# Kernel optimization log

Measured on AMD Instinct MI355X. Metric: run time of the kernel, lower is better.

Reference implementation:

```python
import jax, jax.numpy as jnp
import numpy as np

K_MASK = -2.3819763e+38
ROPE_THETA = 1000000
MROPE_SECTION = (24, 20, 20)
NORM_EPS = 1e-6


def rms_norm(x, w, eps=NORM_EPS):
    dtype = x.dtype
    x32 = x.astype(jnp.float32)
    rms_inv = jax.lax.rsqrt(jnp.mean(x32 * x32, axis=-1, keepdims=True) + eps)
    return w * (x32 * rms_inv).astype(dtype)


def apply_rope(inputs, positions, head_dim, rope_theta=ROPE_THETA, mrope_section=MROPE_SECTION):
    # positions: [3, B, T] (temporal, height, width); inputs: [B, T, heads, head_dim]
    fraction = 2 * jnp.arange(0, head_dim // 2, dtype=jnp.float32) / head_dim
    timescale = rope_theta ** fraction  # [head_dim//2]
    sinusoid = positions[:, :, :, None].astype(jnp.float32) / timescale  # [3,B,T,hd/2]
    freq = sinusoid[0]
    h_idx = jnp.arange(1, mrope_section[1] * 3, 3)
    w_idx = jnp.arange(2, mrope_section[2] * 3, 3)
    freq = freq.at[..., h_idx].set(sinusoid[1][..., h_idx])
    freq = freq.at[..., w_idx].set(sinusoid[2][..., w_idx])
    freq = freq[:, :, None, :]  # [B,T,1,hd/2]
    sin, cos = jnp.sin(freq), jnp.cos(freq)
    first, second = jnp.split(inputs, 2, axis=-1)
    out = jnp.concatenate([first * cos - second * sin, second * cos + first * sin], axis=-1)
    return out.astype(inputs.dtype)


def setup_inputs() -> dict:
    key = jax.random.key(0)
    ks = jax.random.split(key, 6)
    B, T, D, N, K, H = 2, 1024, 2560, 32, 8, 128
    x = jax.random.normal(ks[0], (B, T, D), dtype=jnp.float32)
    positions = jnp.broadcast_to(jnp.arange(T, dtype=jnp.int32), (3, B, T))
    attn_mask = jnp.tril(jnp.ones((T, T), dtype=bool))[None].repeat(B, axis=0)  # causal [B,T,T]
    wq = jax.random.normal(ks[1], (D, N, H), dtype=jnp.float32) * 0.02
    wk = jax.random.normal(ks[2], (D, K, H), dtype=jnp.float32) * 0.02
    wv = jax.random.normal(ks[3], (D, K, H), dtype=jnp.float32) * 0.02
    wo = jax.random.normal(ks[4], (N, H, D), dtype=jnp.float32) * 0.02
    q_norm_w = jnp.ones((H,), dtype=jnp.float32)
    k_norm_w = jnp.ones((H,), dtype=jnp.float32)
    return {"x": x, "positions": positions, "attn_mask": attn_mask, "wq": wq,
            "wk": wk, "wv": wv, "wo": wo, "q_norm_w": q_norm_w, "k_norm_w": k_norm_w}


def reference(x, positions, attn_mask, wq, wk, wv, wo, q_norm_w, k_norm_w):
    head_dim = wo.shape[1]
    scale = head_dim ** -0.5
    q = rms_norm(jnp.einsum('btd,dnh->btnh', x, wq), q_norm_w)
    k = rms_norm(jnp.einsum('bsd,dkh->bskh', x, wk), k_norm_w)
    v = jnp.einsum('bsd,dkh->bskh', x, wv)
    q = apply_rope(q, positions, head_dim)
    k = apply_rope(k, positions, head_dim)
    b, t, qh, d = q.shape
    _, s, kh, _ = k.shape
    q = q.reshape((b, t, kh, qh // kh, d))  # GQA grouping
    attn = jnp.einsum('bthgd,bshd->bhgts', q, k) * scale
    attn = attn.reshape((b, qh, t, s))
    attn = jnp.where(attn_mask[:, None, :, :], attn, K_MASK)
    attn = jax.nn.softmax(attn.astype(jnp.float32), axis=-1).astype(k.dtype)
    attn = attn.reshape((b, kh, qh // kh, t, s))
    qkv = jnp.einsum('bhgts,bshd->bthgd', attn, v).reshape((b, t, qh, d))
    return jnp.einsum('btnh,nhd->btd', qkv, wo)
```

## Files before the change

### kernel.cpp

```cpp
#include <hip/hip_runtime.h>
#include <hip/hip_bf16.h>

typedef __attribute__((ext_vector_type(8))) __bf16 bf8_t;
typedef __attribute__((ext_vector_type(4))) float f32x4;
typedef __attribute__((ext_vector_type(16))) float f32x16;

#define GLOAD16(gptr, lptr)                                                              \
  __builtin_amdgcn_global_load_lds((const __attribute__((address_space(1))) void*)(gptr), \
                                   (__attribute__((address_space(3))) void*)(lptr), 16, 0, 0)

__device__ __forceinline__ unsigned short f2bf(float f) {
  union { float f; unsigned u; } v; v.f = f;
  return (unsigned short)((v.u + 0x7fffu + ((v.u >> 16) & 1u)) >> 16);
}

__device__ __forceinline__ unsigned cvtpk_bf16(float a, float b) {
  unsigned r;
  asm("v_cvt_pk_bf16_f32 %0, %1, %2" : "=v"(r) : "v"(a), "v"(b));
  return r;
}

__global__ void cast_bf16(const float* __restrict__ in, unsigned short* __restrict__ out, int n4) {
  int i = blockIdx.x * blockDim.x + threadIdx.x;
  if (i >= n4) return;
  float4 v = ((const float4*)in)[i];
  ushort4 o;
  o.x = f2bf(v.x); o.y = f2bf(v.y); o.z = f2bf(v.z); o.w = f2bf(v.w);
  ((ushort4*)out)[i] = o;
}

__global__ void tcast(const float* __restrict__ in, unsigned short* __restrict__ out,
                      int R, int C, int ld, int rowOff) {
  __shared__ float tile[32][33];
  int c0 = blockIdx.x * 32, r0 = blockIdx.y * 32;
  int tx = threadIdx.x, ty = threadIdx.y;
#pragma unroll
  for (int i = 0; i < 4; ++i)
    tile[ty + 8 * i][tx] = in[(size_t)(r0 + ty + 8 * i) * C + c0 + tx];
  __syncthreads();
#pragma unroll
  for (int i = 0; i < 4; ++i)
    out[(size_t)(rowOff + c0 + ty + 8 * i) * ld + r0 + tx] = f2bf(tile[tx][ty + 8 * i]);
}

__global__ __launch_bounds__(512, 2) void gemm256(
    const unsigned short* __restrict__ A,
    const unsigned short* __restrict__ Bt,
    float* __restrict__ C0, float* __restrict__ C1,
    int N, int ldk, int Kslice, int nTileN) {
  __shared__ unsigned short SM[4][2][8192];
  int ks = blockIdx.y;
  float* __restrict__ C = ks ? C1 : C0;
  int kbase = ks * Kslice;
  int bm = blockIdx.x / nTileN, bn = blockIdx.x % nTileN;
  int m0 = bm << 8, n0 = bn << 8;
  int tid = threadIdx.x, lane = tid & 63, w = tid >> 6;
  int wm = w >> 2, wn = w & 3;
  int lrow = lane & 15, lch = lane >> 4;
  int srow = tid >> 2, scol = (tid & 3) << 3;
  int nt = Kslice >> 5;

  f32x4 acc[8][4] = {};

  auto stage = [&](int t) {
    int buf = t & 3;
    int k0 = kbase + (t << 5);
    const unsigned short* Ag = A + (size_t)(m0 + srow) * ldk + k0 + scol;
    const unsigned short* Bg = Bt + (size_t)(n0 + srow) * ldk + k0 + scol;
    unsigned short* Al = &SM[buf][0][w << 9];
    unsigned short* Bl = &SM[buf][1][w << 9];
    GLOAD16(Ag, Al);
    GLOAD16(Ag + (size_t)128 * ldk, Al + 4096);
    GLOAD16(Bg, Bl);
    GLOAD16(Bg + (size_t)128 * ldk, Bl + 4096);
  };

  stage(0);
  stage(1);
  for (int t = 0; t < nt; ++t) {
    if (t + 2 < nt) stage(t + 2);
    if (t + 2 < nt)      asm volatile("s_waitcnt vmcnt(8)" ::: "memory");
    else if (t + 1 < nt) asm volatile("s_waitcnt vmcnt(4)" ::: "memory");
    else                 asm volatile("s_waitcnt vmcnt(0)" ::: "memory");
    asm volatile("s_barrier" ::: "memory");
    int buf = t & 3;
    const unsigned short* As = &SM[buf][0][0];
    const unsigned short* Bs = &SM[buf][1][0];
    bf8_t a[8], b[4];
#pragma unroll
    for (int mi = 0; mi < 8; ++mi)
      a[mi] = *(const bf8_t*)(As + ((wm << 7) + (mi << 4) + lrow) * 32 + (lch << 3));
#pragma unroll
    for (int ni = 0; ni < 4; ++ni)
      b[ni] = *(const bf8_t*)(Bs + ((wn << 6) + (ni << 4) + lrow) * 32 + (lch << 3));
    __builtin_amdgcn_s_setprio(1);
#pragma unroll
    for (int mi = 0; mi < 8; ++mi)
#pragma unroll
      for (int ni = 0; ni < 4; ++ni)
        acc[mi][ni] = __builtin_amdgcn_mfma_f32_16x16x32_bf16(a[mi], b[ni], acc[mi][ni], 0, 0, 0);
    __builtin_amdgcn_s_setprio(0);
  }
  int r0 = m0 + (wm << 7) + (lch << 2);
  int c0 = n0 + (wn << 6) + lrow;
#pragma unroll
  for (int mi = 0; mi < 8; ++mi)
#pragma unroll
    for (int ni = 0; ni < 4; ++ni)
#pragma unroll
      for (int r = 0; r < 4; ++r)
        C[(size_t)(r0 + (mi << 4) + r) * N + c0 + (ni << 4)] = acc[mi][ni][r];
}

__global__ void reduce_add(const float4* __restrict__ a, const float4* __restrict__ b,
                           float4* __restrict__ o, int n4) {
  int i = blockIdx.x * blockDim.x + threadIdx.x;
  if (i >= n4) return;
  float4 x = a[i], y = b[i];
  o[i] = make_float4(x.x + y.x, x.y + y.y, x.z + y.z, x.w + y.w);
}

__global__ __launch_bounds__(128) void normrope(
    const float* __restrict__ qkv, const int* __restrict__ positions,
    const float* __restrict__ qw, const float* __restrict__ kw,
    unsigned short* __restrict__ qb, unsigned short* __restrict__ kb,
    unsigned short* __restrict__ vt) {
  int blk = blockIdx.x;
  int hh = blk % 48, bt = blk / 48;
  int b = bt >> 10, t = bt & 1023;
  int tid = threadIdx.x;
  int colbase = (hh < 32) ? (hh << 7) : ((hh < 40) ? (4096 + ((hh - 32) << 7)) : (5120 + ((hh - 40) << 7)));
  float val = qkv[(size_t)bt * 6144 + colbase + tid];
  if (hh >= 40) {
    vt[((size_t)((b * 8 + hh - 40) * 128 + tid)) * 1024 + t] = f2bf(val);
    return;
  }
  __shared__ float red[2];
  __shared__ float xs[128];
  float ss = val * val;
#pragma unroll
  for (int m = 32; m >= 1; m >>= 1) ss += __shfl_xor(ss, m);
  if ((tid & 63) == 0) red[tid >> 6] = ss;
  __syncthreads();
  float rinv = rsqrtf((red[0] + red[1]) * (1.0f / 128.0f) + 1e-6f);
  float wgt = (hh < 32) ? qw[tid] : kw[tid];
  float xn = val * rinv * wgt;
  xs[tid] = xn;
  __syncthreads();
  float other = xs[tid ^ 64];
  int pos = positions[b * 1024 + t];
  int j = tid & 63;
  float ang = (float)pos * exp2f(-(float)j * 0.31143075889569027f);
  float sv = sinf(ang), cv = cosf(ang);
  float outv = (tid < 64) ? (xn * cv - other * sv) : (xn * cv + other * sv);
  unsigned short o = f2bf(outv);
  if (hh < 32) qb[((size_t)((b * 32 + hh) * 1024 + t)) * 128 + tid] = o;
  else kb[((size_t)((b * 8 + hh - 32) * 1024 + t)) * 128 + tid] = o;
}

__global__ __launch_bounds__(256, 2) void attn(
    const unsigned short* __restrict__ qb,
    const unsigned short* __restrict__ kb,
    const unsigned short* __restrict__ vt,
    unsigned short* __restrict__ ob) {
  __shared__ unsigned short Kl[2][64 * 128];
  __shared__ unsigned short Vl[2][128 * 64];
  int bx = blockIdx.x, hq = blockIdx.y, b = blockIdx.z;
  int qt = (bx < 4) ? (7 - bx) : (bx - 4);
  int kvh = hq >> 2;
  int tid = threadIdx.x, lane = tid & 63, w = tid >> 6;
  int qlane = lane & 31, h = lane >> 5;
  int q0 = (qt << 7) + (w << 5);
  int qg = q0 + qlane;
  const unsigned short* kbase = kb + ((size_t)(b * 8 + kvh) << 17);
  const unsigned short* vbase = vt + ((size_t)(b * 8 + kvh) << 17);
  const float c2 = 0.12751744f;

  const unsigned short* qptr = qb + ((size_t)((b * 32 + hq) * 1024 + qg) << 7) + (h << 3);
  bf8_t qf[8];
#pragma unroll
  for (int ds = 0; ds < 8; ++ds) qf[ds] = *(const bf8_t*)(qptr + ds * 16);

  f32x16 o[4] = {};
  float mrun = -3.0e38f, lrun = 0.f;
  int last_st = (q0 + 31) >> 6;
  int nsteps = 2 * qt + 2;

  auto stage = [&](int st, int buf) {
    int s0 = st << 6;
    unsigned short* kd = &Kl[buf][0];
    unsigned short* vd = &Vl[buf][0];
#pragma unroll
    for (int i = 0; i < 4; ++i) {
      int cid = i * 256 + tid;
      int kr = cid >> 4, ksl = cid & 15;
      GLOAD16(kbase + (size_t)(s0 + kr) * 128 + ((ksl ^ (kr & 15)) << 3), kd + cid * 8);
      int vr = cid >> 3, vsl = cid & 7;
      GLOAD16(vbase + (size_t)vr * 1024 + s0 + ((vsl ^ (vr & 7)) << 3), vd + cid * 8);
    }
  };

  stage(0, 0);
  for (int st = 0; st < nsteps; ++st) {
    __syncthreads();
    if (st + 1 < nsteps) stage(st + 1, (st + 1) & 1);
    if (st <= last_st) {
      const char* Kb = (const char*)&Kl[st & 1][0];
      const char* Vb = (const char*)&Vl[st & 1][0];
      f32x16 s0v = {}, s1v = {};
#pragma unroll
      for (int ds = 0; ds < 8; ++ds) {
        int c = ds * 2 + h;
        int r0 = qlane, r1 = 32 + qlane;
        bf8_t k0 = *(const bf8_t*)(Kb + r0 * 256 + ((c ^ (r0 & 15)) << 4));
        bf8_t k1 = *(const bf8_t*)(Kb + r1 * 256 + ((c ^ (r1 & 15)) << 4));
        s0v = __builtin_amdgcn_mfma_f32_32x32x16_bf16(k0, qf[ds], s0v, 0, 0, 0);
        s1v = __builtin_amdgcn_mfma_f32_32x32x16_bf16(k1, qf[ds], s1v, 0, 0, 0);
      }
      bool dm = (st == last_st);
      int kg0 = st << 6;
      float mt = -3.0e38f;
#pragma unroll
      for (int e = 0; e < 16; ++e) {
        int kl = (e & 3) + 8 * (e >> 2) + 4 * h;
        if (dm) {
          if (kg0 + kl > qg) s0v[e] = -3.0e38f;
          if (kg0 + 32 + kl > qg) s1v[e] = -3.0e38f;
        }
        mt = fmaxf(mt, fmaxf(s0v[e], s1v[e]));
      }
      mt = fmaxf(mt, __shfl_xor(mt, 32));
      float mnew = fmaxf(mrun, mt);
      float alpha = exp2f((mrun - mnew) * c2);
      float ls = 0.f;
#pragma unroll
      for (int e = 0; e < 16; ++e) {
        s0v[e] = exp2f((s0v[e] - mnew) * c2);
        s1v[e] = exp2f((s1v[e] - mnew) * c2);
        ls += s0v[e] + s1v[e];
      }
      ls += __shfl_xor(ls, 32);
      lrun = lrun * alpha + ls;
      mrun = mnew;
#pragma unroll
      for (int db = 0; db < 4; ++db)
#pragma unroll
        for (int e = 0; e < 16; ++e) o[db][e] *= alpha;
      bf8_t pf[4];
#pragma unroll
      for (int s = 0; s < 4; ++s) {
        unsigned w00, w01, w10, w11;
        {
          const int B0 = 4 * ((2 * s) & 3);
          if ((2 * s) >> 2) { w00 = cvtpk_bf16(s1v[B0], s1v[B0 + 1]); w01 = cvtpk_bf16(s1v[B0 + 2], s1v[B0 + 3]); }
          else              { w00 = cvtpk_bf16(s0v[B0], s0v[B0 + 1]); w01 = cvtpk_bf16(s0v[B0 + 2], s0v[B0 + 3]); }
        }
        {
          const int B1 = 4 * ((2 * s + 1) & 3);
          if ((2 * s + 1) >> 2) { w10 = cvtpk_bf16(s1v[B1], s1v[B1 + 1]); w11 = cvtpk_bf16(s1v[B1 + 2], s1v[B1 + 3]); }
          else                  { w10 = cvtpk_bf16(s0v[B1], s0v[B1 + 1]); w11 = cvtpk_bf16(s0v[B1 + 2], s0v[B1 + 3]); }
        }
        unsigned sa = h ? w00 : w10, sb = h ? w01 : w11;
        unsigned ra = __shfl_xor(sa, 32), rb = __shfl_xor(sb, 32);
        unsigned ka = h ? w10 : w00, kb2 = h ? w11 : w01;
        unsigned f0 = h ? ra : ka, f1 = h ? rb : kb2;
        unsigned f2 = h ? ka : ra, f3 = h ? kb2 : rb;
        uint4 fv = make_uint4(f0, f1, f2, f3);
        pf[s] = *(bf8_t*)&fv;
      }
#pragma unroll
      for (int db = 0; db < 4; ++db) {
        int vr = (db << 5) + qlane;
#pragma unroll
        for (int s = 0; s < 4; ++s) {
          int c = (s << 1) + h;
          bf8_t vf = *(const bf8_t*)(Vb + vr * 128 + ((c ^ (vr & 7)) << 4));
          o[db] = __builtin_amdgcn_mfma_f32_32x32x16_bf16(vf, pf[s], o[db], 0, 0, 0);
        }
      }
    }
  }

  __syncthreads();
  unsigned short* tb = &Kl[0][0] + (w << 12);
  float inv = 1.0f / lrun;
#pragma unroll
  for (int db = 0; db < 4; ++db)
#pragma unroll
    for (int rq = 0; rq < 4; ++rq) {
      int d0 = (db << 5) + (rq << 3) + (h << 2);
      unsigned lo = ((unsigned)f2bf(o[db][rq * 4 + 1] * inv) << 16) | f2bf(o[db][rq * 4 + 0] * inv);
      unsigned hi = ((unsigned)f2bf(o[db][rq * 4 + 3] * inv) << 16) | f2bf(o[db][rq * 4 + 2] * inv);
      *(uint2*)(tb + qlane * 128 + (d0 ^ ((qlane & 15) << 3))) = make_uint2(lo, hi);
    }
  int rr = lane >> 1, dh = (lane & 1) << 6;
  size_t orow = ((size_t)(b * 1024 + q0 + rr) << 12) + (hq << 7);
#pragma unroll
  for (int i = 0; i < 8; ++i) {
    int d8 = dh + i * 8;
    uint4 vv = *(const uint4*)(tb + rr * 128 + (d8 ^ ((rr & 15) << 3)));
    *(uint4*)(&ob[orow + d8]) = vv;
  }
}

extern "C" void kernel_launch(void* const* d_in, const int* in_sizes, int n_in,
                              void* d_out, int out_size, void* d_ws, size_t ws_size,
                              hipStream_t stream) {
  const float* x = (const float*)d_in[0];
  const int* positions = (const int*)d_in[1];
  const float* wq = (const float*)d_in[3];
  const float* wk = (const float*)d_in[4];
  const float* wv = (const float*)d_in[5];
  const float* wo = (const float*)d_in[6];
  const float* qnw = (const float*)d_in[7];
  const float* knw = (const float*)d_in[8];
  float* out = (float*)d_out;

  char* ws = (char*)d_ws;
  unsigned short* x_bf  = (unsigned short*)(ws);
  unsigned short* wqkvT = (unsigned short*)(ws + 10485760);
  unsigned short* woT   = (unsigned short*)(ws + 41943040);
  float*          qkv   = (float*)(ws + 62914560);
  float*          p0    = (float*)(ws + 62914560);
  float*          p1    = (float*)(ws + 83886080);
  unsigned short* q_bf  = (unsigned short*)(ws + 113246208);
  unsigned short* k_bf  = (unsigned short*)(ws + 130023424);
  unsigned short* vt_bf = (unsigned short*)(ws + 134217728);
  unsigned short* a_bf  = (unsigned short*)(ws + 138412032);

  cast_bf16<<<5120, 256, 0, stream>>>(x, x_bf, 2048 * 2560 / 4);
  tcast<<<dim3(128, 80), dim3(32, 8), 0, stream>>>(wq, wqkvT, 2560, 4096, 2560, 0);
  tcast<<<dim3(32, 80), dim3(32, 8), 0, stream>>>(wk, wqkvT, 2560, 1024, 2560, 4096);
  tcast<<<dim3(32, 80), dim3(32, 8), 0, stream>>>(wv, wqkvT, 2560, 1024, 2560, 5120);
  tcast<<<dim3(80, 128), dim3(32, 8), 0, stream>>>(wo, woT, 4096, 2560, 4096, 0);
  gemm256<<<dim3(8 * 24, 1), 512, 0, stream>>>(x_bf, wqkvT, qkv, nullptr, 6144, 2560, 2560, 24);
  normrope<<<2048 * 48, 128, 0, stream>>>(qkv, positions, qnw, knw, q_bf, k_bf, vt_bf);
  attn<<<dim3(8, 32, 2), 256, 0, stream>>>(q_bf, k_bf, vt_bf, a_bf);
  gemm256<<<dim3(8 * 10, 2), 512, 0, stream>>>(a_bf, woT, p0, p1, 2560, 4096, 2048, 10);
  reduce_add<<<5120, 256, 0, stream>>>((const float4*)p0, (const float4*)p1, (float4*)out,
                                       2048 * 2560 / 4);
}
```

Before: 286.1 us.

## Swizzle GEMM LDS, deepen prefetch, remap workgroups, emit bf16 QKV

The GEMM now XOR-swizzles LDS columns to reduce bank conflicts on fragment reads. It issues the next stage after the barrier with a 3-deep prefetch and remaps block indices across 8 groups, likely for XCD/L2 locality. The QKV projection writes bf16 instead of fp32, halving the intermediate write and the read in normrope. The bf16 rounding of QKV before RMS norm adds a small precision loss, and the new vmcnt accounting with the deeper prefetch needs to stay consistent.

```diff
diff --git a/kernel.cpp b/kernel.cpp
--- a/kernel.cpp
+++ b/kernel.cpp
@@ -12,6 +12,11 @@
 __device__ __forceinline__ unsigned short f2bf(float f) {
   union { float f; unsigned u; } v; v.f = f;
   return (unsigned short)((v.u + 0x7fffu + ((v.u >> 16) & 1u)) >> 16);
+}
+
+__device__ __forceinline__ float bf2f(unsigned short u) {
+  union { unsigned u; float f; } v; v.u = ((unsigned)u) << 16;
+  return v.f;
 }
 
 __device__ __forceinline__ unsigned cvtpk_bf16(float a, float b) {
@@ -47,17 +52,21 @@
     const unsigned short* __restrict__ A,
     const unsigned short* __restrict__ Bt,
     float* __restrict__ C0, float* __restrict__ C1,
+    unsigned short* __restrict__ Cb,
     int N, int ldk, int Kslice, int nTileN) {
   __shared__ unsigned short SM[4][2][8192];
   int ks = blockIdx.y;
-  float* __restrict__ C = ks ? C1 : C0;
   int kbase = ks * Kslice;
-  int bm = blockIdx.x / nTileN, bn = blockIdx.x % nTileN;
+  int nwg = gridDim.x;
+  int bidx = blockIdx.x;
+  int wg = ((bidx & 7) * (nwg >> 3)) + (bidx >> 3);
+  int bm = wg / nTileN, bn = wg % nTileN;
   int m0 = bm << 8, n0 = bn << 8;
   int tid = threadIdx.x, lane = tid & 63, w = tid >> 6;
   int wm = w >> 2, wn = w & 3;
   int lrow = lane & 15, lch = lane >> 4;
-  int srow = tid >> 2, scol = (tid & 3) << 3;
+  int srow = tid >> 2;
+  int scol = ((tid & 3) ^ ((srow >> 1) & 3)) << 3;
   int nt = Kslice >> 5;
 
   f32x4 acc[8][4] = {};
@@ -77,22 +86,27 @@
 
   stage(0);
   stage(1);
+  stage(2);
   for (int t = 0; t < nt; ++t) {
-    if (t + 2 < nt) stage(t + 2);
     if (t + 2 < nt)      asm volatile("s_waitcnt vmcnt(8)" ::: "memory");
     else if (t + 1 < nt) asm volatile("s_waitcnt vmcnt(4)" ::: "memory");
     else                 asm volatile("s_waitcnt vmcnt(0)" ::: "memory");
     asm volatile("s_barrier" ::: "memory");
+    if (t + 3 < nt) stage(t + 3);
     int buf = t & 3;
     const unsigned short* As = &SM[buf][0][0];
     const unsigned short* Bs = &SM[buf][1][0];
     bf8_t a[8], b[4];
 #pragma unroll
-    for (int mi = 0; mi < 8; ++mi)
-      a[mi] = *(const bf8_t*)(As + ((wm << 7) + (mi << 4) + lrow) * 32 + (lch << 3));
-#pragma unroll
-    for (int ni = 0; ni < 4; ++ni)
-      b[ni] = *(const bf8_t*)(Bs + ((wn << 6) + (ni << 4) + lrow) * 32 + (lch << 3));
+    for (int mi = 0; mi < 8; ++mi) {
+      int ar = (wm << 7) + (mi << 4) + lrow;
+      a[mi] = *(const bf8_t*)(As + ar * 32 + ((lch ^ ((ar >> 1) & 3)) << 3));
+    }
+#pragma unroll
+    for (int ni = 0; ni < 4; ++ni) {
+      int br = (wn << 6) + (ni << 4) + lrow;
+      b[ni] = *(const bf8_t*)(Bs + br * 32 + ((lch ^ ((br >> 1) & 3)) << 3));
+    }
     __builtin_amdgcn_s_setprio(1);
 #pragma unroll
     for (int mi = 0; mi < 8; ++mi)
@@ -103,13 +117,24 @@
   }
   int r0 = m0 + (wm << 7) + (lch << 2);
   int c0 = n0 + (wn << 6) + lrow;
-#pragma unroll
-  for (int mi = 0; mi < 8; ++mi)
-#pragma unroll
-    for (int ni = 0; ni < 4; ++ni)
-#pragma unroll
-      for (int r = 0; r < 4; ++r)
-        C[(size_t)(r0 + (mi << 4) + r) * N + c0 + (ni << 4)] = acc[mi][ni][r];
+  if (Cb) {
+#pragma unroll
+    for (int mi = 0; mi < 8; ++mi)
+#pragma unroll
+      for (int ni = 0; ni < 4; ++ni)
+#pragma unroll
+        for (int r = 0; r < 4; ++r)
+          Cb[(size_t)(r0 + (mi << 4) + r) * N + c0 + (ni << 4)] = f2bf(acc[mi][ni][r]);
+  } else {
+    float* __restrict__ C = ks ? C1 : C0;
+#pragma unroll
+    for (int mi = 0; mi < 8; ++mi)
+#pragma unroll
+      for (int ni = 0; ni < 4; ++ni)
+#pragma unroll
+        for (int r = 0; r < 4; ++r)
+          C[(size_t)(r0 + (mi << 4) + r) * N + c0 + (ni << 4)] = acc[mi][ni][r];
+  }
 }
 
 __global__ void reduce_add(const float4* __restrict__ a, const float4* __restrict__ b,
@@ -121,7 +146,7 @@
 }
 
 __global__ __launch_bounds__(128) void normrope(
-    const float* __restrict__ qkv, const int* __restrict__ positions,
+    const unsigned short* __restrict__ qkv, const int* __restrict__ positions,
     const float* __restrict__ qw, const float* __restrict__ kw,
     unsigned short* __restrict__ qb, unsigned short* __restrict__ kb,
     unsigned short* __restrict__ vt) {
@@ -130,7 +155,7 @@
   int b = bt >> 10, t = bt & 1023;
   int tid = threadIdx.x;
   int colbase = (hh < 32) ? (hh << 7) : ((hh < 40) ? (4096 + ((hh - 32) << 7)) : (5120 + ((hh - 40) << 7)));
-  float val = qkv[(size_t)bt * 6144 + colbase + tid];
+  float val = bf2f(qkv[(size_t)bt * 6144 + colbase + tid]);
   if (hh >= 40) {
     vt[((size_t)((b * 8 + hh - 40) * 128 + tid)) * 1024 + t] = f2bf(val);
     return;
@@ -320,7 +345,7 @@
   unsigned short* x_bf  = (unsigned short*)(ws);
   unsigned short* wqkvT = (unsigned short*)(ws + 10485760);
   unsigned short* woT   = (unsigned short*)(ws + 41943040);
-  float*          qkv   = (float*)(ws + 62914560);
+  unsigned short* qkvb  = (unsigned short*)(ws + 62914560);
   float*          p0    = (float*)(ws + 62914560);
   float*          p1    = (float*)(ws + 83886080);
   unsigned short* q_bf  = (unsigned short*)(ws + 113246208);
@@ -333,10 +358,11 @@
   tcast<<<dim3(32, 80), dim3(32, 8), 0, stream>>>(wk, wqkvT, 2560, 1024, 2560, 4096);
   tcast<<<dim3(32, 80), dim3(32, 8), 0, stream>>>(wv, wqkvT, 2560, 1024, 2560, 5120);
   tcast<<<dim3(80, 128), dim3(32, 8), 0, stream>>>(wo, woT, 4096, 2560, 4096, 0);
-  gemm256<<<dim3(8 * 24, 1), 512, 0, stream>>>(x_bf, wqkvT, qkv, nullptr, 6144, 2560, 2560, 24);
-  normrope<<<2048 * 48, 128, 0, stream>>>(qkv, positions, qnw, knw, q_bf, k_bf, vt_bf);
+  gemm256<<<dim3(8 * 24, 1), 512, 0, stream>>>(x_bf, wqkvT, nullptr, nullptr, qkvb,
+                                               6144, 2560, 2560, 24);
+  normrope<<<2048 * 48, 128, 0, stream>>>(qkvb, positions, qnw, knw, q_bf, k_bf, vt_bf);
   attn<<<dim3(8, 32, 2), 256, 0, stream>>>(q_bf, k_bf, vt_bf, a_bf);
-  gemm256<<<dim3(8 * 10, 2), 512, 0, stream>>>(a_bf, woT, p0, p1, 2560, 4096, 2048, 10);
+  gemm256<<<dim3(8 * 10, 2), 512, 0, stream>>>(a_bf, woT, p0, p1, nullptr, 2560, 4096, 2048, 10);
   reduce_add<<<5120, 256, 0, stream>>>((const float4*)p0, (const float4*)p1, (float4*)out,
                                        2048 * 2560 / 4);
 }
```

After: 286.3 us. No clear change (+0.1%).
